# Optimization experiments

Hardware: AMD Instinct MI355X
Metric: run time of the kernel (lower is better)

The kernel has to match this reference:

```python
import jax, jax.numpy as jnp
import numpy as np

NPOINT = 1024
NSAMPLE = 32
RADIUS = 0.2


def index_points2(points, idx):
    # points: (B,N,D), idx: (B,S) -> (B,S,D)
    return jnp.take_along_axis(points, idx[..., None], axis=1)


def index_points3(points, idx):
    # points: (B,N,D), idx: (B,S,K) -> (B,S,K,D)
    B, S, K = idx.shape
    flat = jnp.take_along_axis(points, idx.reshape(B, S * K)[..., None], axis=1)
    return flat.reshape(B, S, K, points.shape[-1])


def farthest_point_sampling(xyz, npoint):
    # xyz: (B,N,3) -> (B,npoint) int32 indices. First point deterministic (index 0).
    B, N, _ = xyz.shape
    first = jnp.zeros((B,), jnp.int32)
    chosen = jnp.zeros((B, npoint), jnp.int32).at[:, 0].set(first)
    first_xyz = index_points2(xyz, first[:, None])[:, 0, :]
    dist_min = jnp.sum((xyz - first_xyz[:, None, :]) ** 2, axis=-1)  # (B,N)

    def body(i, carry):
        chosen, dist_min = carry
        far = jnp.argmax(dist_min, axis=-1).astype(jnp.int32)  # (B,)
        far_xyz = index_points2(xyz, far[:, None])[:, 0, :]
        d = jnp.sum((xyz - far_xyz[:, None, :]) ** 2, axis=-1)
        return chosen.at[:, i].set(far), jnp.minimum(dist_min, d)

    chosen, _ = jax.lax.fori_loop(1, npoint, body, (chosen, dist_min))
    return chosen


def query_ball_point(radius, nsample, xyz, new_xyz):
    # (B,S,N) squared distances; out-of-ball -> inf; take nsample nearest (stable argsort).
    dist = jnp.sum((new_xyz[:, :, None, :] - xyz[:, None, :, :]) ** 2, axis=-1)
    dist_m = jnp.where(dist <= radius ** 2, dist, jnp.inf)
    return jnp.argsort(dist_m, axis=-1)[:, :, :nsample]


def mlp2(x, Wa, ba, Wb, bb, act2):
    h = jax.nn.relu(x @ Wa + ba)
    return act2(h @ Wb + bb)


def reference(xyz, features, W1, b1, W2, b2, W3, b3, W4, b4):
    fps_idx = farthest_point_sampling(xyz, NPOINT)          # (B,S)
    new_xyz = index_points2(xyz, fps_idx)                   # (B,S,3)
    group_idx = query_ball_point(RADIUS, NSAMPLE, xyz, new_xyz)  # (B,S,K)
    grouped_xyz = index_points3(xyz, group_idx)             # (B,S,K,3)
    grouped_xyz_norm = grouped_xyz - new_xyz[:, :, None, :]
    grouped_feats = index_points3(features, group_idx)      # (B,S,K,C)
    f_in = jnp.concatenate([grouped_xyz_norm, grouped_feats], axis=-1)
    f_prime = mlp2(f_in, W1, b1, W2, b2, jax.nn.relu)       # (B,S,K,H)
    f_mean = jnp.mean(f_prime, axis=2, keepdims=True)
    w_in = jnp.concatenate([grouped_xyz_norm, f_prime - f_mean], axis=-1)
    alpha = mlp2(w_in, W3, b3, W4, b4, jax.nn.sigmoid)      # (B,S,K,H)
    f_out = jnp.sum(alpha * f_prime, axis=2)                # (B,S,H)
    return new_xyz, f_out


def setup_inputs() -> dict:
    key = jax.random.key(0)
    ks = jax.random.split(key, 8)
    B, N, C, H = 16, 4096, 64, 128
    xyz = jax.random.uniform(ks[0], (B, N, 3), dtype=jnp.float32)
    features = jax.random.normal(ks[1], (B, N, C), dtype=jnp.float32)
    s = 0.1
    return {
        "xyz": xyz,
        "features": features,
        "W1": jax.random.normal(ks[2], (3 + C, H), dtype=jnp.float32) * s,
        "b1": jnp.zeros((H,), jnp.float32),
        "W2": jax.random.normal(ks[3], (H, H), dtype=jnp.float32) * s,
        "b2": jnp.zeros((H,), jnp.float32),
        "W3": jax.random.normal(ks[4], (3 + H, H), dtype=jnp.float32) * s,
        "b3": jnp.zeros((H,), jnp.float32),
        "W4": jax.random.normal(ks[5], (H, H), dtype=jnp.float32) * s,
        "b4": jnp.zeros((H,), jnp.float32),
    }
```

## Files before the change

### kernel.cpp

```cpp
#include <hip/hip_runtime.h>

typedef unsigned short u16;
typedef unsigned int   u32;
typedef unsigned long long u64;
typedef short s8v __attribute__((ext_vector_type(8)));
typedef float f4v __attribute__((ext_vector_type(4)));
typedef float f2v __attribute__((ext_vector_type(2)));

#define STRIDE 168
#define CAP 512
#define OFF_G1 0
#define OFF_G2 12288
#define OFF_G3 28672
#define OFF_G4 49152

__device__ __forceinline__ float bf2f(u16 u){ return __uint_as_float(((u32)u)<<16); }
__device__ __forceinline__ u16 f2bf(float f){
  u32 u = __float_as_uint(f);
  return (u16)((u + 0x7FFFu + ((u>>16)&1u)) >> 16);
}
__device__ __forceinline__ float sqd(float ax,float ay,float az,float bx,float by,float bz){
  float dx=ax-bx, dy=ay-by, dz=az-bz;
  return __fadd_rn(__fadd_rn(__fmul_rn(dx,dx),__fmul_rn(dy,dy)),__fmul_rn(dz,dz));
}

#define WMAX_STEP(v, CTRL) { \
  u32 _t = (u32)__builtin_amdgcn_update_dpp(0, (int)(v), CTRL, 0xf, 0xf, false); \
  (v) = (v) > _t ? (v) : _t; }
#define QMAX64(k, CTRL) { \
  u32 _lo=(u32)(k), _hi=(u32)((k)>>32); \
  u32 _plo=(u32)__builtin_amdgcn_update_dpp(0,(int)_lo,CTRL,0xf,0xf,true); \
  u32 _phi=(u32)__builtin_amdgcn_update_dpp(0,(int)_hi,CTRL,0xf,0xf,true); \
  u64 _o=((u64)_phi<<32)|_plo; (k) = (k)>_o ? (k) : _o; }

__global__ __launch_bounds__(256) void fps_kernel(const float* __restrict__ xyz,
                                                  float* __restrict__ newxyz){
  __shared__ __align__(16) float S[4096*3];
  __shared__ u64 red[2][4];
  const int b = blockIdx.x, tid = threadIdx.x;
  const int lane = tid & 63, wv = tid >> 6;
  const float* xb = xyz + (size_t)b*4096*3;
  #pragma unroll
  for(int j=0;j<12;j++) ((float4*)S)[j*256+tid] = ((const float4*)xb)[j*256+tid];
  __syncthreads();
  f2v X[8],Y[8],Z[8],DM[8];
  const float x0=S[0], y0=S[1], z0=S[2];
  {
    #pragma clang fp contract(off)
    const f2v fx2={x0,x0}, fy2={y0,y0}, fz2={z0,z0};
    #pragma unroll
    for(int k2=0;k2<8;k2++){
      int p0 = tid*16 + 2*k2;
      X[k2] = (f2v){S[p0*3],   S[p0*3+3]};
      Y[k2] = (f2v){S[p0*3+1], S[p0*3+4]};
      Z[k2] = (f2v){S[p0*3+2], S[p0*3+5]};
      f2v dx=X[k2]-fx2, dy=Y[k2]-fy2, dz=Z[k2]-fz2;
      DM[k2] = (dx*dx + dy*dy) + dz*dz;
    }
  }
  if(tid==0){
    size_t o=(size_t)b*1024*3;
    newxyz[o]=x0; newxyz[o+1]=y0; newxyz[o+2]=z0;
  }
  for(int i=1;i<1024;i++){
    float vm = DM[0][0]; int jm = 0;
    #pragma unroll
    for(int j=1;j<16;j++){
      float dj = DM[j>>1][j&1];
      bool g = dj > vm; vm = g ? dj : vm; jm = g ? j : jm;
    }
    u32 w = __float_as_uint(vm);
    WMAX_STEP(w, 0x111); WMAX_STEP(w, 0x112); WMAX_STEP(w, 0x114);
    WMAX_STEP(w, 0x118); WMAX_STEP(w, 0x142); WMAX_STEP(w, 0x143);
    u32 wm = (u32)__builtin_amdgcn_readlane((int)w, 63);
    u64 msk = __ballot(__float_as_uint(vm) == wm);
    int ldr = __ffsll((unsigned long long)msk) - 1;
    int pj  = __builtin_amdgcn_readlane(jm, ldr);
    int p   = (wv*64 + ldr)*16 + pj;
    if(lane==0) red[i&1][wv] = ((u64)wm<<32) | (u32)(~(u32)p);
    __syncthreads();
    u64 k = red[i&1][lane&3];
    QMAX64(k, 0xB1); QMAX64(k, 0x4E);
    int far = (int)(~(u32)k) & 4095;
    float fx=S[far*3], fy=S[far*3+1], fz=S[far*3+2];
    if(tid==0){
      size_t o=((size_t)b*1024+i)*3;
      newxyz[o]=fx; newxyz[o+1]=fy; newxyz[o+2]=fz;
    }
    {
      #pragma clang fp contract(off)
      const f2v fx2={fx,fx}, fy2={fy,fy}, fz2={fz,fz};
      #pragma unroll
      for(int k2=0;k2<8;k2++){
        f2v dx=X[k2]-fx2, dy=Y[k2]-fy2, dz=Z[k2]-fz2;
        f2v s = (dx*dx + dy*dy) + dz*dz;
        DM[k2] = __builtin_elementwise_min(DM[k2], s);
      }
    }
  }
}

__global__ __launch_bounds__(256) void swz_kernel(const float* __restrict__ W1,const float* __restrict__ W2,
                                                  const float* __restrict__ W3,const float* __restrict__ W4,
                                                  u16* __restrict__ wsw){
  int T = blockIdx.x*256 + threadIdx.x;
  const float* W; int rel, base, kind;
  if(T < 1536){ rel=T;      base=OFF_G1; W=W1; kind=0; }
  else if(T < 3584){ rel=T-1536; base=OFF_G2; W=W2; kind=1; }
  else if(T < 6144){ rel=T-3584; base=OFF_G3; W=W3; kind=0; }
  else         { rel=T-6144; base=OFF_G4; W=W4; kind=1; }
  int chunk=rel>>6, lane=rel&63, c=chunk>>3, t=chunk&7, quad=lane>>4, l15=lane&15;
  u16 v[8];
  #pragma unroll
  for(int j=0;j<8;j++){
    int kp = c*32 + quad*8 + j, n = t*16 + l15;
    int src = (kind==0) ? (kp<3 ? kp : (kp>=32 ? kp-29 : -1)) : kp;
    v[j] = (src<0) ? (u16)0 : f2bf(W[src*128 + n]);
  }
  int4 o;
  o.x=(int)((u32)v[0]|((u32)v[1]<<16)); o.y=(int)((u32)v[2]|((u32)v[3]<<16));
  o.z=(int)((u32)v[4]|((u32)v[5]<<16)); o.w=(int)((u32)v[6]|((u32)v[7]<<16));
  *(int4*)&wsw[base + rel*8] = o;
}

__device__ __forceinline__ void zero_C(f4v C[2][8]){
  #pragma unroll
  for(int mt=0;mt<2;mt++)
    #pragma unroll
    for(int t=0;t<8;t++) C[mt][t] = (f4v){0.f,0.f,0.f,0.f};
}
__device__ __forceinline__ void load_bias(const float* bsrc,int l15,float bb[8]){
  #pragma unroll
  for(int t=0;t<8;t++) bb[t]=bsrc[t*16+l15];
}
template<int KC>
__device__ __forceinline__ void run_gemm(const u16* A, const u16* BW,
                                         int lane,int l15,int quad, f4v C[2][8]){
  s8v af[2][KC];
  #pragma unroll
  for(int mt=0;mt<2;mt++)
    #pragma unroll
    for(int c=0;c<KC;c++)
      af[mt][c] = *(const s8v*)&A[(mt*16+l15)*STRIDE + c*32 + quad*8];
  #pragma unroll
  for(int t=0;t<8;t++){
    #pragma unroll
    for(int c=0;c<KC;c++){
      s8v bw = *(const s8v*)&BW[((c*8+t)*64 + lane)*8];
      C[0][t] = __builtin_amdgcn_mfma_f32_16x16x32_bf16(af[0][c],bw,C[0][t],0,0,0);
      C[1][t] = __builtin_amdgcn_mfma_f32_16x16x32_bf16(af[1][c],bw,C[1][t],0,0,0);
    }
  }
}
__device__ __forceinline__ void store_act(u16* A,int l15,int quad,f4v C[2][8],const float bb[8]){
  #pragma unroll
  for(int mt=0;mt<2;mt++)
    #pragma unroll
    for(int t=0;t<8;t++)
      #pragma unroll
      for(int r=0;r<4;r++){
        float v = fmaxf(C[mt][t][r]+bb[t], 0.f);
        A[(mt*16+quad*4+r)*STRIDE + t*16 + l15] = f2bf(v);
      }
}
__device__ __forceinline__ void write_xyz_chunk0(u16* A,int lane,float xn,float yn,float zn){
  if(lane<32){
    u16* row=&A[lane*STRIDE];
    row[0]=f2bf(xn); row[1]=f2bf(yn); row[2]=f2bf(zn); row[3]=0;
    #pragma unroll
    for(int q=0;q<7;q++) *(u64*)&row[4+q*4] = 0ull;
  }
}

__global__ __launch_bounds__(256,2) void mlp_kernel(const float* __restrict__ xyz,
    const float* __restrict__ feats, const u16* __restrict__ wsw,
    const float* __restrict__ b1,const float* __restrict__ b2,const float* __restrict__ b3,const float* __restrict__ b4,
    const float* __restrict__ newxyz, float* __restrict__ fout){
  __shared__ __align__(16) u16 Abuf[4][32*STRIDE];
  __shared__ u64 Bcand[4][CAP];
  __shared__ int selbuf[4][32];
  const int tid=threadIdx.x, wv=tid>>6, lane=tid&63, quad=lane>>4, l15=lane&15;
  const int widx = blockIdx.x*4 + wv, b = widx>>10;
  u16* A = Abuf[wv];
  const float* xb = xyz + (size_t)b*4096*3;
  const float cx=newxyz[widx*3], cy=newxyz[widx*3+1], cz=newxyz[widx*3+2];

  {
    u64* Bc = Bcand[wv];
    int* sel = selbuf[wv];
    const u64 lt = (1ull<<lane)-1ull;
    int base=0;
    for(int kk=0;kk<64;kk++){
      int p = kk*64 + lane;
      float d = sqd(cx,cy,cz, xb[p*3],xb[p*3+1],xb[p*3+2]);
      bool in = (d <= 0.04f);
      u64 m = __ballot(in);
      if(in){ int pos = base + __popcll(m&lt); if(pos<CAP) Bc[pos] = ((u64)__float_as_uint(d)<<32)|(u32)p; }
      base += __popcll(m);
    }
    int cnt = base>CAP ? CAP : base;
    if(cnt > 32){
      for(int c=lane; c<cnt; c+=64){
        u64 key = Bc[c]; int r=0;
        for(int t2=0;t2<cnt;t2++) r += (Bc[t2] < key) ? 1 : 0;
        if(r < 32) sel[r] = (int)(u32)key;
      }
    } else {
      for(int c=lane; c<cnt; c+=64) sel[c] = (int)(u32)Bc[c];
      int need = 32 - cnt, b2 = 0;
      for(int kk=0; kk<64 && b2<need; kk++){
        int p = kk*64 + lane;
        float d = sqd(cx,cy,cz, xb[p*3],xb[p*3+1],xb[p*3+2]);
        bool o = !(d <= 0.04f);
        u64 m = __ballot(o);
        if(o){ int pos = b2 + __popcll(m&lt); if(pos<need) sel[cnt+pos] = p; }
        b2 += __popcll(m);
      }
    }
  }
  const int* sel = selbuf[wv];
  const int gi_f = sel[lane>>1] & 4095;
  const int gi_x = sel[lane & 31] & 4095;

  {
    int r2=lane>>1, h=lane&1;
    const float* fs = feats + ((size_t)b*4096 + gi_f)*64 + h*32;
    u16* fd = &A[r2*STRIDE + 32 + h*32];
    #pragma unroll
    for(int j=0;j<8;j++){
      float4 v4 = ((const float4*)fs)[j];
      u64 pk4 = (u64)f2bf(v4.x) | ((u64)f2bf(v4.y)<<16)
              | ((u64)f2bf(v4.z)<<32) | ((u64)f2bf(v4.w)<<48);
      *(u64*)&fd[j*4] = pk4;
    }
  }
  float xn=0.f,yn=0.f,zn=0.f;
  if(lane<32){
    const float* xp = xb + (size_t)gi_x*3;
    xn = xp[0]-cx; yn = xp[1]-cy; zn = xp[2]-cz;
  }
  write_xyz_chunk0(A,lane,xn,yn,zn);
  __syncthreads();

  f4v C[2][8]; float bb[8];
  zero_C(C); load_bias(b1,l15,bb);
  run_gemm<3>(A, wsw+OFF_G1, lane,l15,quad, C);
  store_act(A,l15,quad,C,bb);
  __syncthreads();
  zero_C(C); load_bias(b2,l15,bb);
  run_gemm<4>(A, wsw+OFF_G2, lane,l15,quad, C);
  float fp[2][8][4]; float mean[8];
  #pragma unroll
  for(int t=0;t<8;t++){
    float s=0.f;
    #pragma unroll
    for(int mt=0;mt<2;mt++)
      #pragma unroll
      for(int r=0;r<4;r++){
        float v = fmaxf(C[mt][t][r]+bb[t], 0.f);
        fp[mt][t][r]=v; s+=v;
      }
    s += __shfl_xor(s,16); s += __shfl_xor(s,32);
    mean[t] = s*0.03125f;
  }
  #pragma unroll
  for(int mt=0;mt<2;mt++)
    #pragma unroll
    for(int t=0;t<8;t++)
      #pragma unroll
      for(int r=0;r<4;r++)
        A[(mt*16+quad*4+r)*STRIDE + 32 + t*16 + l15] = f2bf(fp[mt][t][r]-mean[t]);
  write_xyz_chunk0(A,lane,xn,yn,zn);
  __syncthreads();
  zero_C(C); load_bias(b3,l15,bb);
  run_gemm<5>(A, wsw+OFF_G3, lane,l15,quad, C);
  store_act(A,l15,quad,C,bb);
  __syncthreads();
  zero_C(C); load_bias(b4,l15,bb);
  run_gemm<4>(A, wsw+OFF_G4, lane,l15,quad, C);
  float* fo = fout + (size_t)widx*128;
  #pragma unroll
  for(int t=0;t<8;t++){
    float part=0.f;
    #pragma unroll
    for(int mt=0;mt<2;mt++)
      #pragma unroll
      for(int r=0;r<4;r++){
        float pre = C[mt][t][r]+bb[t];
        float a = 1.f/(1.f+__expf(-pre));
        part += a*fp[mt][t][r];
      }
    part += __shfl_xor(part,16); part += __shfl_xor(part,32);
    if(quad==0) fo[t*16+l15] = part;
  }
}

extern "C" void kernel_launch(void* const* d_in, const int* in_sizes, int n_in,
                              void* d_out, int out_size, void* d_ws, size_t ws_size,
                              hipStream_t stream){
  (void)in_sizes; (void)n_in; (void)out_size; (void)ws_size;
  const float* xyz   = (const float*)d_in[0];
  const float* feats = (const float*)d_in[1];
  const float* W1 = (const float*)d_in[2]; const float* b1 = (const float*)d_in[3];
  const float* W2 = (const float*)d_in[4]; const float* b2 = (const float*)d_in[5];
  const float* W3 = (const float*)d_in[6]; const float* b3 = (const float*)d_in[7];
  const float* W4 = (const float*)d_in[8]; const float* b4 = (const float*)d_in[9];
  float* out = (float*)d_out;
  float* newxyz = out;
  float* fout   = out + 16*1024*3;
  u16* wsw = (u16*)d_ws;

  hipLaunchKernelGGL(swz_kernel, dim3(32),   dim3(256), 0, stream, W1,W2,W3,W4, wsw);
  hipLaunchKernelGGL(fps_kernel, dim3(16),   dim3(256), 0, stream, xyz, newxyz);
  hipLaunchKernelGGL(mlp_kernel, dim3(4096), dim3(256), 0, stream,
                     xyz, feats, wsw, b1,b2,b3,b4, newxyz, fout);
}
```

Before: 1.024 ms.

## Pass winner coordinates through shared reduction slots in FPS and raise MLP occupancy

In the FPS loop, each wave's leader lane now writes its winning point's coordinates, taken from registers, together with its key into shared memory. After the barrier every thread reduces the four candidates directly, with no DPP 64-bit reduction and no dependent LDS lookup into the point array. This shortens the serial critical path of each of the 1023 iterations. Separately, the MLP kernel's candidate buffer CAP is halved and launch bounds are raised to 3 blocks per CU for higher occupancy, at the cost of register pressure and possible overflow if a ball ever holds more than 256 candidates.

```diff
diff --git a/kernel.cpp b/kernel.cpp
--- a/kernel.cpp
+++ b/kernel.cpp
@@ -8,7 +8,7 @@
 typedef float f2v __attribute__((ext_vector_type(2)));
 
 #define STRIDE 168
-#define CAP 512
+#define CAP 256
 #define OFF_G1 0
 #define OFF_G2 12288
 #define OFF_G3 28672
@@ -27,16 +27,11 @@
 #define WMAX_STEP(v, CTRL) { \
   u32 _t = (u32)__builtin_amdgcn_update_dpp(0, (int)(v), CTRL, 0xf, 0xf, false); \
   (v) = (v) > _t ? (v) : _t; }
-#define QMAX64(k, CTRL) { \
-  u32 _lo=(u32)(k), _hi=(u32)((k)>>32); \
-  u32 _plo=(u32)__builtin_amdgcn_update_dpp(0,(int)_lo,CTRL,0xf,0xf,true); \
-  u32 _phi=(u32)__builtin_amdgcn_update_dpp(0,(int)_hi,CTRL,0xf,0xf,true); \
-  u64 _o=((u64)_phi<<32)|_plo; (k) = (k)>_o ? (k) : _o; }
 
 __global__ __launch_bounds__(256) void fps_kernel(const float* __restrict__ xyz,
                                                   float* __restrict__ newxyz){
   __shared__ __align__(16) float S[4096*3];
-  __shared__ u64 red[2][4];
+  __shared__ __align__(32) float red[2][4][8];
   const int b = blockIdx.x, tid = threadIdx.x;
   const int lane = tid & 63, wv = tid >> 6;
   const float* xb = xyz + (size_t)b*4096*3;
@@ -69,20 +64,43 @@
       float dj = DM[j>>1][j&1];
       bool g = dj > vm; vm = g ? dj : vm; jm = g ? j : jm;
     }
+    int idx = jm>>1;
+    f2v xa=(idx&1)?X[1]:X[0], xb2=(idx&1)?X[3]:X[2], xc=(idx&1)?X[5]:X[4], xd=(idx&1)?X[7]:X[6];
+    f2v ya=(idx&1)?Y[1]:Y[0], yb2=(idx&1)?Y[3]:Y[2], yc=(idx&1)?Y[5]:Y[4], yd=(idx&1)?Y[7]:Y[6];
+    f2v za=(idx&1)?Z[1]:Z[0], zb2=(idx&1)?Z[3]:Z[2], zc=(idx&1)?Z[5]:Z[4], zd=(idx&1)?Z[7]:Z[6];
+    f2v xe=(idx&2)?xb2:xa, xf=(idx&2)?xd:xc;
+    f2v ye=(idx&2)?yb2:ya, yf=(idx&2)?yd:yc;
+    f2v ze=(idx&2)?zb2:za, zf=(idx&2)?zd:zc;
+    f2v xg=(idx&4)?xf:xe, yg=(idx&4)?yf:ye, zg=(idx&4)?zf:ze;
+    float cxx=(jm&1)?xg[1]:xg[0], cyy=(jm&1)?yg[1]:yg[0], czz=(jm&1)?zg[1]:zg[0];
     u32 w = __float_as_uint(vm);
     WMAX_STEP(w, 0x111); WMAX_STEP(w, 0x112); WMAX_STEP(w, 0x114);
     WMAX_STEP(w, 0x118); WMAX_STEP(w, 0x142); WMAX_STEP(w, 0x143);
     u32 wm = (u32)__builtin_amdgcn_readlane((int)w, 63);
     u64 msk = __ballot(__float_as_uint(vm) == wm);
     int ldr = __ffsll((unsigned long long)msk) - 1;
-    int pj  = __builtin_amdgcn_readlane(jm, ldr);
-    int p   = (wv*64 + ldr)*16 + pj;
-    if(lane==0) red[i&1][wv] = ((u64)wm<<32) | (u32)(~(u32)p);
+    if(lane==ldr){
+      int p = (wv*64 + lane)*16 + jm;
+      float* rr = red[i&1][wv];
+      rr[0]=__uint_as_float(~(u32)p); rr[1]=__uint_as_float(wm);
+      rr[2]=cxx; rr[3]=cyy; rr[4]=czz;
+    }
     __syncthreads();
-    u64 k = red[i&1][lane&3];
-    QMAX64(k, 0xB1); QMAX64(k, 0x4E);
-    int far = (int)(~(u32)k) & 4095;
-    float fx=S[far*3], fy=S[far*3+1], fz=S[far*3+2];
+    const float* r0=red[i&1][0]; const float* r1=red[i&1][1];
+    const float* r2=red[i&1][2]; const float* r3=red[i&1][3];
+    float4 q0=*(const float4*)r0, q1=*(const float4*)r1,
+           q2=*(const float4*)r2, q3=*(const float4*)r3;
+    float z0v=r0[4], z1v=r1[4], z2v=r2[4], z3v=r3[4];
+    u64 k0=((u64)__float_as_uint(q0.y)<<32)|__float_as_uint(q0.x);
+    u64 k1=((u64)__float_as_uint(q1.y)<<32)|__float_as_uint(q1.x);
+    u64 k2=((u64)__float_as_uint(q2.y)<<32)|__float_as_uint(q2.x);
+    u64 k3=((u64)__float_as_uint(q3.y)<<32)|__float_as_uint(q3.x);
+    bool g1 = k1>k0; u64 ka=g1?k1:k0;
+    float ax=g1?q1.z:q0.z, ay=g1?q1.w:q0.w, az=g1?z1v:z0v;
+    bool g2 = k3>k2; u64 kb=g2?k3:k2;
+    float bx=g2?q3.z:q2.z, by=g2?q3.w:q2.w, bz=g2?z3v:z2v;
+    bool g3 = kb>ka;
+    float fx=g3?bx:ax, fy=g3?by:ay, fz=g3?bz:az;
     if(tid==0){
       size_t o=((size_t)b*1024+i)*3;
       newxyz[o]=fx; newxyz[o+1]=fy; newxyz[o+2]=fz;
@@ -91,10 +109,10 @@
       #pragma clang fp contract(off)
       const f2v fx2={fx,fx}, fy2={fy,fy}, fz2={fz,fz};
       #pragma unroll
-      for(int k2=0;k2<8;k2++){
-        f2v dx=X[k2]-fx2, dy=Y[k2]-fy2, dz=Z[k2]-fz2;
+      for(int k2c=0;k2c<8;k2c++){
+        f2v dx=X[k2c]-fx2, dy=Y[k2c]-fy2, dz=Z[k2c]-fz2;
         f2v s = (dx*dx + dy*dy) + dz*dz;
-        DM[k2] = __builtin_elementwise_min(DM[k2], s);
+        DM[k2c] = __builtin_elementwise_min(DM[k2c], s);
       }
     }
   }
@@ -172,7 +190,7 @@
   }
 }
 
-__global__ __launch_bounds__(256,2) void mlp_kernel(const float* __restrict__ xyz,
+__global__ __launch_bounds__(256,3) void mlp_kernel(const float* __restrict__ xyz,
     const float* __restrict__ feats, const u16* __restrict__ wsw,
     const float* __restrict__ b1,const float* __restrict__ b2,const float* __restrict__ b3,const float* __restrict__ b4,
     const float* __restrict__ newxyz, float* __restrict__ fout){
```

New measurement: 1.323 ms. 29.2% more time.
